# Optimization experiments

Measured on AMD Instinct MI355X. Metric: run time of the kernel, lower is better.

Reference implementation:

```python
import jax, jax.numpy as jnp
from jax import lax
import numpy as np

LRELU_SLOPE = 0.2
DEMOD_EPS = 1e-8


def _mod_conv(x, style, weight, bias, demodulate, pad):
    """StyleGAN2 modulated conv via grouped conv (groups = batch).
    x: [B,Cin,H,W]; style: [B,Cin]; weight: [Cout,Cin,kh,kw]; bias: [Cout]."""
    B, Cin, H, W = x.shape
    Cout, _, kh, kw = weight.shape
    # per-sample modulated weight [B,Cout,Cin,kh,kw]
    wt = weight[None] * style[:, None, :, None, None]
    if demodulate:
        wt = wt / jnp.sqrt(jnp.sum(wt ** 2, axis=(2, 3, 4), keepdims=True) + DEMOD_EPS)
    out = lax.conv_general_dilated(
        x.reshape(1, B * Cin, H, W),
        wt.reshape(B * Cout, Cin, kh, kw),
        window_strides=(1, 1),
        padding=[(pad, pad), (pad, pad)],
        dimension_numbers=('NCHW', 'OIHW', 'NCHW'),
        feature_group_count=B,
    )
    return out.reshape(B, Cout, H, W) + bias[None, :, None, None]


def setup_inputs() -> dict:
    key = jax.random.key(0)
    ks = jax.random.split(key, 16)
    B, Cin, Cout, Wd, H = 4, 512, 256, 512, 64
    f32 = jnp.float32
    d = {
        'x': jax.random.normal(ks[0], (B, Cin, H, H), f32),
        'w': jax.random.normal(ks[1], (B, Wd), f32),
        # conv1: Cin->Cout 3x3
        'w1': jax.random.normal(ks[2], (Cout, Cin, 3, 3), f32) / np.float32(np.sqrt(Cin * 9)),
        'b1': jax.random.normal(ks[3], (Cout,), f32) * 0.01,
        'a1w': jax.random.normal(ks[4], (Cin, Wd), f32) / np.float32(np.sqrt(Wd)),
        'a1b': jnp.ones((Cin,), f32),
        # conv2: Cout->Cout 3x3
        'w2': jax.random.normal(ks[5], (Cout, Cout, 3, 3), f32) / np.float32(np.sqrt(Cout * 9)),
        'b2': jax.random.normal(ks[6], (Cout,), f32) * 0.01,
        'a2w': jax.random.normal(ks[7], (Cout, Wd), f32) / np.float32(np.sqrt(Wd)),
        'a2b': jnp.ones((Cout,), f32),
        # to_rgb: Cout->3 1x1, no demodulation
        'w3': jax.random.normal(ks[8], (3, Cout, 1, 1), f32) / np.float32(np.sqrt(Cout)),
        'b3': jax.random.normal(ks[9], (3,), f32) * 0.01,
        'a3w': jax.random.normal(ks[10], (Cout, Wd), f32) / np.float32(np.sqrt(Wd)),
        'a3b': jnp.ones((Cout,), f32),
    }
    return d


def reference(x, w, w1, b1, a1w, a1b, w2, b2, a2w, a2b, w3, b3, a3w, a3b):
    B, C, H, W = x.shape
    # nn.Upsample(scale_factor=2, mode='bilinear', align_corners=False) == half-pixel bilinear
    xu = jax.image.resize(x, (B, C, 2 * H, 2 * W), method='bilinear')
    s1 = w @ a1w.T + a1b                      # affine -> per-sample style [B,Cin]
    h = jax.nn.leaky_relu(_mod_conv(xu, s1, w1, b1, True, 1), LRELU_SLOPE)
    s2 = w @ a2w.T + a2b
    h = jax.nn.leaky_relu(_mod_conv(h, s2, w2, b2, True, 1), LRELU_SLOPE)
    s3 = w @ a3w.T + a3b
    rgb = jax.nn.leaky_relu(_mod_conv(h, s3, w3, b3, False, 0), LRELU_SLOPE)
    return (h, rgb)
```

## Files before the change

kernel.cpp:

```cpp
#include <hip/hip_runtime.h>
#include <stdint.h>

typedef __attribute__((ext_vector_type(8))) short bhalf8;
typedef __attribute__((ext_vector_type(4))) float fx4;

__device__ __forceinline__ unsigned short f2bf(float f) {
    unsigned u = __builtin_bit_cast(unsigned, f);
    unsigned r = (u + 0x7fffu + ((u >> 16) & 1u)) >> 16;
    return (unsigned short)r;
}
__device__ __forceinline__ float bf2f(unsigned short h) {
    unsigned u = ((unsigned)h) << 16;
    return __builtin_bit_cast(float, u);
}
__device__ __forceinline__ float lrelu(float v) { return v > 0.f ? v : 0.2f * v; }

typedef __attribute__((address_space(1))) void as1_void;
typedef __attribute__((address_space(3))) void as3_void;
__device__ __forceinline__ void gl_lds16(const void* g, void* l) {
    __builtin_amdgcn_global_load_lds((as1_void*)(void*)g, (as3_void*)l, 16, 0, 0);
}

__global__ __launch_bounds__(256) void style_kernel(
    const float* __restrict__ w,
    const float* __restrict__ a1w, const float* __restrict__ a1b,
    const float* __restrict__ a2w, const float* __restrict__ a2b,
    const float* __restrict__ a3w, const float* __restrict__ a3b,
    float* __restrict__ s1, float* __restrict__ s2, float* __restrict__ s3)
{
    int gw = blockIdx.x * 4 + (threadIdx.x >> 6);
    int lane = threadIdx.x & 63;
    int b = gw >> 10, r = gw & 1023;
    const float* arow; const float* abias; float* dst;
    if (r < 512)      { arow = a1w + (size_t)r * 512;        abias = a1b + r;       dst = s1 + b * 512 + r; }
    else if (r < 768) { int rr = r - 512; arow = a2w + (size_t)rr * 512; abias = a2b + rr; dst = s2 + b * 256 + rr; }
    else              { int rr = r - 768; arow = a3w + (size_t)rr * 512; abias = a3b + rr; dst = s3 + b * 256 + rr; }
    const float* wrow = w + b * 512;
    float acc = 0.f;
    #pragma unroll
    for (int j = 0; j < 8; ++j) {
        int c = lane + j * 64;
        acc += wrow[c] * arow[c];
    }
    #pragma unroll
    for (int off = 32; off; off >>= 1) acc += __shfl_down(acc, off, 64);
    if (lane == 0) *dst = acc + *abias;
}

__global__ __launch_bounds__(256) void demod_kernel(
    const float* __restrict__ w1, const float* __restrict__ w2,
    const float* __restrict__ s1, const float* __restrict__ s2,
    float* __restrict__ d1, float* __restrict__ d2)
{
    int blk = blockIdx.x;
    int conv = blk >> 10, b = (blk >> 8) & 3, o = blk & 255;
    int t = threadIdx.x;
    int cin = conv ? 256 : 512;
    const float* s = conv ? (s2 + b * 256) : (s1 + b * 512);
    const float* row = (conv ? w2 : w1) + (size_t)o * cin * 9;
    __shared__ float sv[512];
    for (int i = t; i < cin; i += 256) { float v = s[i]; sv[i] = v * v; }
    __syncthreads();
    float sum = 0.f;
    int n = cin * 9;
    for (int k = t; k < n; k += 256) {
        float v = row[k];
        sum += v * v * sv[k / 9];
    }
    #pragma unroll
    for (int off = 32; off; off >>= 1) sum += __shfl_down(sum, off, 64);
    __shared__ float red[4];
    if ((t & 63) == 0) red[t >> 6] = sum;
    __syncthreads();
    if (t == 0) {
        float tot = red[0] + red[1] + red[2] + red[3];
        (conv ? d2 : d1)[b * 256 + o] = rsqrtf(tot + 1e-8f);
    }
}

__global__ __launch_bounds__(256) void pack_kernel(
    const float* __restrict__ w1, const float* __restrict__ w2,
    unsigned short* __restrict__ wp1, unsigned short* __restrict__ wp2)
{
    int tid = blockIdx.x * 256 + threadIdx.x;
    const int N1 = 1179648, N2 = 589824;
    if (tid < N1) {
        int e = tid & 7, m = (tid >> 3) & 127, kh = (tid >> 10) & 3;
        int dx = (tid >> 12) % 3, ic = (tid / 12288) & 15;
        int dy = (tid / 196608) % 3, mblk = tid / 589824;
        int o = mblk * 128 + m, ci = ic * 32 + kh * 8 + e;
        wp1[tid] = f2bf(w1[((size_t)o * 512 + ci) * 9 + dy * 3 + dx]);
    } else if (tid < N1 + N2) {
        int t2 = tid - N1;
        int e = t2 & 7, m = (t2 >> 3) & 127, kh = (t2 >> 10) & 3;
        int dx = (t2 >> 12) % 3, ic = (t2 / 12288) & 7;
        int dy = (t2 / 98304) % 3, mblk = t2 / 294912;
        int o = mblk * 128 + m, ci = ic * 32 + kh * 8 + e;
        wp2[t2] = f2bf(w2[((size_t)o * 256 + ci) * 9 + dy * 3 + dx]);
    }
}

__global__ __launch_bounds__(256) void upsample_kernel(
    const float* __restrict__ x, const float* __restrict__ s1,
    unsigned short* __restrict__ xu)
{
    __shared__ float Lt[3][64][68];
    const int bid = blockIdx.x;
    const int cch = bid & 7, k = (bid >> 3) & 63, b = bid >> 9;
    const int c0 = cch * 64;
    const int t = threadIdx.x;

    {
        const int px4 = t & 15, cc4 = t >> 4;
        #pragma unroll
        for (int r = 0; r < 3; ++r) {
            int sy = k - 1 + r; sy = sy < 0 ? 0 : (sy > 63 ? 63 : sy);
            float4 v[4];
            #pragma unroll
            for (int j = 0; j < 4; ++j)
                v[j] = *(const float4*)&x[((size_t)(b * 512 + c0 + cc4 * 4 + j) * 64 + sy) * 64 + px4 * 4];
            #pragma unroll
            for (int o = 0; o < 4; ++o) {
                fx4 w4;
                w4[0] = ((const float*)&v[0])[o];
                w4[1] = ((const float*)&v[1])[o];
                w4[2] = ((const float*)&v[2])[o];
                w4[3] = ((const float*)&v[3])[o];
                *(fx4*)&Lt[r][px4 * 4 + o][cc4 * 4] = w4;
            }
        }
    }
    __syncthreads();

    const int oct = t & 7, xob = t >> 3;
    float sty[8];
    #pragma unroll
    for (int j = 0; j < 8; ++j) sty[j] = s1[b * 512 + c0 + oct * 8 + j];

    #pragma unroll
    for (int half = 0; half < 2; ++half) {
        const int yo = 2 * k + half;
        const int rA = half ? 1 : 0, rB = rA + 1;
        const float wyA = half ? 0.75f : 0.25f, wyB = half ? 0.25f : 0.75f;
        #pragma unroll
        for (int i = 0; i < 4; ++i) {
            const int xo = xob + i * 32;
            const int kk = xo >> 1;
            int sx0, sx1; float wx0, wx1;
            if ((xo & 1) == 0) { sx0 = kk > 0 ? kk - 1 : 0; sx1 = kk; wx0 = 0.25f; wx1 = 0.75f; }
            else               { sx0 = kk; sx1 = kk < 63 ? kk + 1 : 63; wx0 = 0.75f; wx1 = 0.25f; }
            unsigned pk[4];
            #pragma unroll
            for (int h = 0; h < 2; ++h) {
                const fx4 a0 = *(const fx4*)&Lt[rA][sx0][oct * 8 + h * 4];
                const fx4 a1 = *(const fx4*)&Lt[rA][sx1][oct * 8 + h * 4];
                const fx4 b0 = *(const fx4*)&Lt[rB][sx0][oct * 8 + h * 4];
                const fx4 b1 = *(const fx4*)&Lt[rB][sx1][oct * 8 + h * 4];
                #pragma unroll
                for (int j2 = 0; j2 < 2; ++j2) {
                    float v0 = wyA * (wx0 * a0[j2 * 2]     + wx1 * a1[j2 * 2])
                             + wyB * (wx0 * b0[j2 * 2]     + wx1 * b1[j2 * 2]);
                    float v1 = wyA * (wx0 * a0[j2 * 2 + 1] + wx1 * a1[j2 * 2 + 1])
                             + wyB * (wx0 * b0[j2 * 2 + 1] + wx1 * b1[j2 * 2 + 1]);
                    v0 *= sty[h * 4 + j2 * 2];
                    v1 *= sty[h * 4 + j2 * 2 + 1];
                    pk[h * 2 + j2] = (unsigned)f2bf(v0) | ((unsigned)f2bf(v1) << 16);
                }
            }
            *(int4*)&xu[((size_t)(b * 128 + yo) * 128 + xo) * 512 + c0 + oct * 8] =
                make_int4(pk[0], pk[1], pk[2], pk[3]);
        }
    }
}

template<int CIN, bool IS_CONV2>
__global__ __launch_bounds__(512, 4) void conv3x3_kernel(
    const unsigned short* __restrict__ inp,
    const unsigned short* __restrict__ wpack,
    const float* __restrict__ dvec,
    const float* __restrict__ bias,
    const float* __restrict__ post,
    unsigned short* __restrict__ outmod,
    float* __restrict__ outf)
{
    constexpr int NIC = CIN / 32;
    __shared__ __attribute__((aligned(16))) short Alds[2][12288];
    __shared__ __attribute__((aligned(16))) short Blds[4][128][32];
    const int tid = threadIdx.x;
    const int lane = tid & 63;
    const int wvi = tid >> 6;
    const int bid = blockIdx.x;
    const int y0 = (bid & 63) << 1;
    const int mblk = (bid >> 6) & 1;
    const int b = bid >> 7;
    const int wm = (wvi >> 2) * 64;
    const int row = (wvi >> 1) & 1;
    const int wn = (wvi & 1) * 64;
    const int lhi = lane >> 4;
    const int llo = lane & 15;

    const int xg = tid >> 2, i8 = tid & 3;
    const int i8s = i8 ^ ((xg >> 1) & 3);

    fx4 acc[4][4];
    #pragma unroll
    for (int mt = 0; mt < 4; ++mt)
        #pragma unroll
        for (int nt = 0; nt < 4; ++nt) acc[mt][nt] = (fx4){0.f, 0.f, 0.f, 0.f};

    auto stageB = [&](int ic) {
        #pragma unroll
        for (int rr = 0; rr < 4; ++rr) {
            const int yy = y0 - 1 + rr;
            char* dstB = (char*)&Blds[rr][0][0] + tid * 16;
            if ((unsigned)yy < 128u) {
                gl_lds16(inp + ((size_t)(b * 128 + yy) * 128 + xg) * CIN + ic * 32 + i8s * 8, dstB);
            } else {
                *(int4*)dstB = make_int4(0, 0, 0, 0);
            }
        }
    };
    auto stageA = [&](int ic, int dy, int buf) {
        const unsigned short* asrc = wpack + ((size_t)(mblk * 3 + dy) * NIC + ic) * 12288;
        #pragma unroll
        for (int j = 0; j < 3; ++j) {
            int g = tid + j * 512;
            gl_lds16(asrc + (size_t)g * 8, (char*)&Alds[buf][0] + g * 16);
        }
    };

    stageB(0);
    stageA(0, 0, 0);
    __syncthreads();

    int par = 0;
    for (int ic = 0; ic < NIC; ++ic) {
        #pragma unroll
        for (int dy = 0; dy < 3; ++dy) {
            const bool last = (ic == NIC - 1) && (dy == 2);
            if (!last) {
                const int nic = (dy == 2) ? ic + 1 : ic;
                const int ndy = (dy == 2) ? 0 : dy + 1;
                stageA(nic, ndy, par ^ 1);
            }
            const short* Ab = &Alds[par][0];
            const short* Brow = &Blds[row + dy][0][0];
            #pragma unroll
            for (int dx = 0; dx < 3; ++dx) {
                bhalf8 af[4], bfr[4];
                #pragma unroll
                for (int mt = 0; mt < 4; ++mt)
                    af[mt] = *(const bhalf8*)&Ab[dx * 4096 + (lhi * 128 + wm + mt * 16 + llo) * 8];
                #pragma unroll
                for (int nt = 0; nt < 4; ++nt) {
                    const int s = wn + nt * 16 + llo + dx;
                    if ((nt == 0 && dx == 0) || (nt == 3 && dx == 2)) {
                        const bool edge = (s == 0) || (s == 129);
                        const int sp = edge ? 0 : (s - 1);
                        const int key = (sp >> 1) & 3;
                        bhalf8 v = *(const bhalf8*)&Brow[sp * 32 + ((lhi ^ key) << 3)];
                        bhalf8 z = {0, 0, 0, 0, 0, 0, 0, 0};
                        bfr[nt] = edge ? z : v;
                    } else {
                        const int sp = s - 1;
                        const int key = (sp >> 1) & 3;
                        bfr[nt] = *(const bhalf8*)&Brow[sp * 32 + ((lhi ^ key) << 3)];
                    }
                }
                __builtin_amdgcn_s_setprio(1);
                #pragma unroll
                for (int mt = 0; mt < 4; ++mt)
                    #pragma unroll
                    for (int nt = 0; nt < 4; ++nt)
                        acc[mt][nt] = __builtin_amdgcn_mfma_f32_16x16x32_bf16(
                            af[mt], bfr[nt], acc[mt][nt], 0, 0, 0);
                __builtin_amdgcn_s_setprio(0);
            }
            if (dy == 2 && ic + 1 < NIC) {
                __syncthreads();
                stageB(ic + 1);
            }
            if (!last) __syncthreads();
            par ^= 1;
        }
    }

    const int y = y0 + row;
    #pragma unroll
    for (int mt = 0; mt < 4; ++mt) {
        const int o0 = mblk * 128 + wm + mt * 16 + lhi * 4;
        const fx4 d4 = *(const fx4*)(dvec + b * 256 + o0);
        const fx4 bb4 = *(const fx4*)(bias + o0);
        const fx4 p4 = *(const fx4*)(post + b * 256 + o0);
        #pragma unroll
        for (int nt = 0; nt < 4; ++nt) {
            const int xo = wn + nt * 16 + llo;
            unsigned lo = 0, hi = 0;
            #pragma unroll
            for (int r = 0; r < 4; ++r) {
                float v = acc[mt][nt][r] * d4[r] + bb4[r];
                v = lrelu(v);
                if (IS_CONV2)
                    outf[(((size_t)b * 256 + o0 + r) * 128 + y) * 128 + xo] = v;
                unsigned short ub = f2bf(v * p4[r]);
                if (r < 2) lo |= (unsigned)ub << (16 * r);
                else       hi |= (unsigned)ub << (16 * (r - 2));
            }
            *(uint2*)&outmod[((size_t)(b * 128 + y) * 128 + xo) * 256 + o0] = make_uint2(lo, hi);
        }
    }
}

__global__ __launch_bounds__(256) void rgb_kernel(
    const unsigned short* __restrict__ hs3,
    const float* __restrict__ w3, const float* __restrict__ b3,
    float* __restrict__ out)
{
    __shared__ float wl[768];
    int t = threadIdx.x;
    for (int i = t; i < 768; i += 256) wl[i] = w3[i];
    __syncthreads();
    int p = blockIdx.x * 64 + (t >> 2);
    int q = t & 3;
    const unsigned short* src = hs3 + (size_t)p * 256 + q * 64;
    float a0 = 0.f, a1 = 0.f, a2 = 0.f;
    #pragma unroll
    for (int c8 = 0; c8 < 64; c8 += 8) {
        int4 pk = *(const int4*)(src + c8);
        #pragma unroll
        for (int qq = 0; qq < 4; ++qq) {
            unsigned uu = ((const unsigned*)&pk)[qq];
            float ve = bf2f((unsigned short)(uu & 0xffffu));
            float vo = bf2f((unsigned short)(uu >> 16));
            int c = q * 64 + c8 + qq * 2;
            a0 += ve * wl[c] + vo * wl[c + 1];
            a1 += ve * wl[256 + c] + vo * wl[256 + c + 1];
            a2 += ve * wl[512 + c] + vo * wl[512 + c + 1];
        }
    }
    a0 += __shfl_xor(a0, 1, 64); a0 += __shfl_xor(a0, 2, 64);
    a1 += __shfl_xor(a1, 1, 64); a1 += __shfl_xor(a1, 2, 64);
    a2 += __shfl_xor(a2, 1, 64); a2 += __shfl_xor(a2, 2, 64);
    int b = p >> 14, yx = p & 16383;
    if (q < 3) {
        float v = (q == 0) ? a0 : (q == 1) ? a1 : a2;
        out[((size_t)b * 3 + q) * 16384 + yx] = lrelu(v + b3[q]);
    }
}

extern "C" void kernel_launch(void* const* d_in, const int* in_sizes, int n_in,
                              void* d_out, int out_size, void* d_ws, size_t ws_size,
                              hipStream_t stream) {
    const float* x   = (const float*)d_in[0];
    const float* w   = (const float*)d_in[1];
    const float* w1  = (const float*)d_in[2];
    const float* b1  = (const float*)d_in[3];
    const float* a1w = (const float*)d_in[4];
    const float* a1b = (const float*)d_in[5];
    const float* w2  = (const float*)d_in[6];
    const float* b2  = (const float*)d_in[7];
    const float* a2w = (const float*)d_in[8];
    const float* a2b = (const float*)d_in[9];
    const float* w3  = (const float*)d_in[10];
    const float* b3  = (const float*)d_in[11];
    const float* a3w = (const float*)d_in[12];
    const float* a3b = (const float*)d_in[13];

    char* ws = (char*)d_ws;
    unsigned short* xu  = (unsigned short*)(ws);
    unsigned short* hs3 = (unsigned short*)(ws);
    unsigned short* t1  = (unsigned short*)(ws + 67108864);
    unsigned short* wp1 = (unsigned short*)(ws + 100663296);
    unsigned short* wp2 = (unsigned short*)(ws + 103022592);
    float* s1 = (float*)(ws + 104202240);
    float* s2 = (float*)(ws + 104210432);
    float* s3 = (float*)(ws + 104214528);
    float* d1 = (float*)(ws + 104218624);
    float* d2 = (float*)(ws + 104222720);

    float* h_out   = (float*)d_out;
    float* rgb_out = h_out + 16777216;

    style_kernel<<<1024, 256, 0, stream>>>(w, a1w, a1b, a2w, a2b, a3w, a3b, s1, s2, s3);
    demod_kernel<<<2048, 256, 0, stream>>>(w1, w2, s1, s2, d1, d2);
    pack_kernel<<<6912, 256, 0, stream>>>(w1, w2, wp1, wp2);
    upsample_kernel<<<2048, 256, 0, stream>>>(x, s1, xu);
    conv3x3_kernel<512, false><<<512, 512, 0, stream>>>(xu, wp1, d1, b1, s2, t1, nullptr);
    conv3x3_kernel<256, true><<<512, 512, 0, stream>>>(t1, wp2, d2, b2, s3, hs3, h_out);
    rgb_kernel<<<1024, 256, 0, stream>>>(hs3, w3, b3, rgb_out);
}
```

Before: 361.9 us.

## Pipeline conv weight/input staging per dx with vmcnt-counted waits and ring buffers

Result: slower. 792.3 us (+118.9%).

```diff
diff --git a/kernel.cpp b/kernel.cpp
--- a/kernel.cpp
+++ b/kernel.cpp
@@ -184,8 +184,8 @@
     float* __restrict__ outf)
 {
     constexpr int NIC = CIN / 32;
-    __shared__ __attribute__((aligned(16))) short Alds[2][12288];
-    __shared__ __attribute__((aligned(16))) short Blds[4][128][32];
+    __shared__ __attribute__((aligned(16))) short Alds[3][4096];
+    __shared__ __attribute__((aligned(16))) short Blds[6][128][32];
     const int tid = threadIdx.x;
     const int lane = tid & 63;
     const int wvi = tid >> 6;
@@ -198,59 +198,91 @@
     const int wn = (wvi & 1) * 64;
     const int lhi = lane >> 4;
     const int llo = lane & 15;
+    const int e0 = (y0 == 0) ? 1 : 0;
+    const int e1 = (y0 == 126) ? 1 : 0;
 
     const int xg = tid >> 2, i8 = tid & 3;
     const int i8s = i8 ^ ((xg >> 1) & 3);
 
+#define WAITVM(N) asm volatile("s_waitcnt vmcnt(" #N ") lgkmcnt(0)" ::: "memory")
+#define CBAR()    asm volatile("" ::: "memory")
+
+    auto stageA1 = [&](int qic, int qdy, int qdx, int slot) {
+        const unsigned short* asrc = wpack + ((size_t)(mblk * 3 + qdy) * NIC + qic) * 12288
+                                           + qdx * 4096;
+        gl_lds16(asrc + (size_t)tid * 8, (char*)&Alds[slot][0] + tid * 16);
+    };
+    auto stageB1 = [&](int icn, int rr, int slot) {
+        const int yy = y0 - 1 + rr;
+        char* dstB = (char*)&Blds[slot][0][0] + tid * 16;
+        if ((unsigned)yy < 128u) {
+            gl_lds16(inp + ((size_t)(b * 128 + yy) * 128 + xg) * CIN + icn * 32 + i8s * 8, dstB);
+        } else {
+            *(int4*)dstB = make_int4(0, 0, 0, 0);
+        }
+    };
+
     fx4 acc[4][4];
     #pragma unroll
     for (int mt = 0; mt < 4; ++mt)
         #pragma unroll
         for (int nt = 0; nt < 4; ++nt) acc[mt][nt] = (fx4){0.f, 0.f, 0.f, 0.f};
 
-    auto stageB = [&](int ic) {
-        #pragma unroll
-        for (int rr = 0; rr < 4; ++rr) {
-            const int yy = y0 - 1 + rr;
-            char* dstB = (char*)&Blds[rr][0][0] + tid * 16;
-            if ((unsigned)yy < 128u) {
-                gl_lds16(inp + ((size_t)(b * 128 + yy) * 128 + xg) * CIN + ic * 32 + i8s * 8, dstB);
-            } else {
-                *(int4*)dstB = make_int4(0, 0, 0, 0);
-            }
-        }
-    };
-    auto stageA = [&](int ic, int dy, int buf) {
-        const unsigned short* asrc = wpack + ((size_t)(mblk * 3 + dy) * NIC + ic) * 12288;
-        #pragma unroll
-        for (int j = 0; j < 3; ++j) {
-            int g = tid + j * 512;
-            gl_lds16(asrc + (size_t)g * 8, (char*)&Alds[buf][0] + g * 16);
-        }
-    };
-
-    stageB(0);
-    stageA(0, 0, 0);
-    __syncthreads();
-
-    int par = 0;
+    stageA1(0, 0, 0, 0); CBAR();
+    stageA1(0, 0, 1, 1); CBAR();
+    stageB1(0, 0, 0); CBAR();
+    stageB1(0, 1, 1); CBAR();
+    stageB1(0, 2, 2); CBAR();
+    stageB1(0, 3, 3); CBAR();
+
+    int bbase = 0;
     for (int ic = 0; ic < NIC; ++ic) {
+        const bool lastic = (ic == NIC - 1);
         #pragma unroll
         for (int dy = 0; dy < 3; ++dy) {
-            const bool last = (ic == NIC - 1) && (dy == 2);
-            if (!last) {
-                const int nic = (dy == 2) ? ic + 1 : ic;
-                const int ndy = (dy == 2) ? 0 : dy + 1;
-                stageA(nic, ndy, par ^ 1);
-            }
-            const short* Ab = &Alds[par][0];
-            const short* Brow = &Blds[row + dy][0][0];
             #pragma unroll
             for (int dx = 0; dx < 3; ++dx) {
+                int n;
+                if (ic == 0 && dy == 0 && dx == 0) n = 2 - e1;
+                else if (lastic) n = (dy == 2 && dx == 2) ? 0 : 1;
+                else if (dx == 0) n = 1;
+                else if (dy == 0) n = 3 - e0;
+                else if (dy == 1) n = 2;
+                else n = 2 - e1;
+                if (n == 0) WAITVM(0);
+                else if (n == 1) WAITVM(1);
+                else if (n == 2) WAITVM(2);
+                else WAITVM(3);
+                __builtin_amdgcn_s_barrier();
+                __builtin_amdgcn_sched_barrier(0);
+                {
+                    const int poff = 3 * dy + dx + 2;
+                    if (!(lastic && dy == 2 && dx >= 1)) {
+                        const int qic = ic + (poff >= 9 ? 1 : 0);
+                        const int qoff = poff >= 9 ? poff - 9 : poff;
+                        stageA1(qic, qoff / 3, qoff % 3, (dx + 2) % 3);
+                        CBAR();
+                    }
+                }
+                if (dx == 0 && !lastic) {
+                    if (dy == 0) {
+                        int s4 = bbase + 4; if (s4 >= 6) s4 -= 6;
+                        int s5 = bbase + 5; if (s5 >= 6) s5 -= 6;
+                        stageB1(ic + 1, 0, s4); CBAR();
+                        stageB1(ic + 1, 1, s5); CBAR();
+                    } else if (dy == 1) {
+                        stageB1(ic + 1, 2, bbase); CBAR();
+                    } else {
+                        int s1b = bbase + 1; if (s1b >= 6) s1b -= 6;
+                        stageB1(ic + 1, 3, s1b); CBAR();
+                    }
+                }
+                int sb = bbase + row + dy; if (sb >= 6) sb -= 6;
+                const short* Brow = &Blds[sb][0][0];
                 bhalf8 af[4], bfr[4];
                 #pragma unroll
                 for (int mt = 0; mt < 4; ++mt)
-                    af[mt] = *(const bhalf8*)&Ab[dx * 4096 + (lhi * 128 + wm + mt * 16 + llo) * 8];
+                    af[mt] = *(const bhalf8*)&Alds[dx][(lhi * 128 + wm + mt * 16 + llo) * 8];
                 #pragma unroll
                 for (int nt = 0; nt < 4; ++nt) {
                     const int s = wn + nt * 16 + llo + dx;
@@ -276,14 +308,11 @@
                             af[mt], bfr[nt], acc[mt][nt], 0, 0, 0);
                 __builtin_amdgcn_s_setprio(0);
             }
-            if (dy == 2 && ic + 1 < NIC) {
-                __syncthreads();
-                stageB(ic + 1);
-            }
-            if (!last) __syncthreads();
-            par ^= 1;
-        }
-    }
+        }
+        bbase += 4; if (bbase >= 6) bbase -= 6;
+    }
+#undef WAITVM
+#undef CBAR
 
     const int y = y0 + row;
     #pragma unroll
```

## Fuse to_rgb 1x1 projection into conv2 epilogue with atomic partial sums

Applied to the files above, without the earlier changes.

Measured after the change: 354.7 us. 1.02x faster.

```diff
diff --git a/kernel.cpp b/kernel.cpp
--- a/kernel.cpp
+++ b/kernel.cpp
@@ -181,7 +181,9 @@
     const float* __restrict__ bias,
     const float* __restrict__ post,
     unsigned short* __restrict__ outmod,
-    float* __restrict__ outf)
+    float* __restrict__ outf,
+    const float* __restrict__ w3,
+    float* __restrict__ rgbpart)
 {
     constexpr int NIC = CIN / 32;
     __shared__ __attribute__((aligned(16))) short Alds[2][12288];
@@ -286,66 +288,73 @@
     }
 
     const int y = y0 + row;
-    #pragma unroll
-    for (int mt = 0; mt < 4; ++mt) {
-        const int o0 = mblk * 128 + wm + mt * 16 + lhi * 4;
-        const fx4 d4 = *(const fx4*)(dvec + b * 256 + o0);
-        const fx4 bb4 = *(const fx4*)(bias + o0);
-        const fx4 p4 = *(const fx4*)(post + b * 256 + o0);
+    if constexpr (!IS_CONV2) {
+        #pragma unroll
+        for (int mt = 0; mt < 4; ++mt) {
+            const int o0 = mblk * 128 + wm + mt * 16 + lhi * 4;
+            const fx4 d4 = *(const fx4*)(dvec + b * 256 + o0);
+            const fx4 bb4 = *(const fx4*)(bias + o0);
+            const fx4 p4 = *(const fx4*)(post + b * 256 + o0);
+            #pragma unroll
+            for (int nt = 0; nt < 4; ++nt) {
+                const int xo = wn + nt * 16 + llo;
+                unsigned lo = 0, hi = 0;
+                #pragma unroll
+                for (int r = 0; r < 4; ++r) {
+                    float v = acc[mt][nt][r] * d4[r] + bb4[r];
+                    v = lrelu(v);
+                    unsigned short ub = f2bf(v * p4[r]);
+                    if (r < 2) lo |= (unsigned)ub << (16 * r);
+                    else       hi |= (unsigned)ub << (16 * (r - 2));
+                }
+                *(uint2*)&outmod[((size_t)(b * 128 + y) * 128 + xo) * 256 + o0] = make_uint2(lo, hi);
+            }
+        }
+    } else {
         #pragma unroll
         for (int nt = 0; nt < 4; ++nt) {
             const int xo = wn + nt * 16 + llo;
-            unsigned lo = 0, hi = 0;
-            #pragma unroll
-            for (int r = 0; r < 4; ++r) {
-                float v = acc[mt][nt][r] * d4[r] + bb4[r];
-                v = lrelu(v);
-                if (IS_CONV2)
+            float pq0 = 0.f, pq1 = 0.f, pq2 = 0.f;
+            #pragma unroll
+            for (int mt = 0; mt < 4; ++mt) {
+                const int o0 = mblk * 128 + wm + mt * 16 + lhi * 4;
+                const fx4 d4 = *(const fx4*)(dvec + b * 256 + o0);
+                const fx4 bb4 = *(const fx4*)(bias + o0);
+                const fx4 p4 = *(const fx4*)(post + b * 256 + o0);
+                const fx4 wq0 = *(const fx4*)(w3 + o0);
+                const fx4 wq1 = *(const fx4*)(w3 + 256 + o0);
+                const fx4 wq2 = *(const fx4*)(w3 + 512 + o0);
+                #pragma unroll
+                for (int r = 0; r < 4; ++r) {
+                    float v = acc[mt][nt][r] * d4[r] + bb4[r];
+                    v = lrelu(v);
                     outf[(((size_t)b * 256 + o0 + r) * 128 + y) * 128 + xo] = v;
-                unsigned short ub = f2bf(v * p4[r]);
-                if (r < 2) lo |= (unsigned)ub << (16 * r);
-                else       hi |= (unsigned)ub << (16 * (r - 2));
-            }
-            *(uint2*)&outmod[((size_t)(b * 128 + y) * 128 + xo) * 256 + o0] = make_uint2(lo, hi);
-        }
-    }
-}
-
-__global__ __launch_bounds__(256) void rgb_kernel(
-    const unsigned short* __restrict__ hs3,
-    const float* __restrict__ w3, const float* __restrict__ b3,
+                    const float hv = v * p4[r];
+                    pq0 += wq0[r] * hv;
+                    pq1 += wq1[r] * hv;
+                    pq2 += wq2[r] * hv;
+                }
+            }
+            pq0 += __shfl_xor(pq0, 16, 64); pq0 += __shfl_xor(pq0, 32, 64);
+            pq1 += __shfl_xor(pq1, 16, 64); pq1 += __shfl_xor(pq1, 32, 64);
+            pq2 += __shfl_xor(pq2, 16, 64); pq2 += __shfl_xor(pq2, 32, 64);
+            if (lhi == 0) {
+                float* rp = rgbpart + (size_t)b * 49152 + (size_t)y * 128 + xo;
+                atomicAdd(rp, pq0);
+                atomicAdd(rp + 16384, pq1);
+                atomicAdd(rp + 32768, pq2);
+            }
+        }
+    }
+}
+
+__global__ __launch_bounds__(256) void rgb_finish_kernel(
+    const float* __restrict__ part, const float* __restrict__ b3,
     float* __restrict__ out)
 {
-    __shared__ float wl[768];
-    int t = threadIdx.x;
-    for (int i = t; i < 768; i += 256) wl[i] = w3[i];
-    __syncthreads();
-    int p = blockIdx.x * 64 + (t >> 2);
-    int q = t & 3;
-    const unsigned short* src = hs3 + (size_t)p * 256 + q * 64;
-    float a0 = 0.f, a1 = 0.f, a2 = 0.f;
-    #pragma unroll
-    for (int c8 = 0; c8 < 64; c8 += 8) {
-        int4 pk = *(const int4*)(src + c8);
-        #pragma unroll
-        for (int qq = 0; qq < 4; ++qq) {
-            unsigned uu = ((const unsigned*)&pk)[qq];
-            float ve = bf2f((unsigned short)(uu & 0xffffu));
-            float vo = bf2f((unsigned short)(uu >> 16));
-            int c = q * 64 + c8 + qq * 2;
-            a0 += ve * wl[c] + vo * wl[c + 1];
-            a1 += ve * wl[256 + c] + vo * wl[256 + c + 1];
-            a2 += ve * wl[512 + c] + vo * wl[512 + c + 1];
-        }
-    }
-    a0 += __shfl_xor(a0, 1, 64); a0 += __shfl_xor(a0, 2, 64);
-    a1 += __shfl_xor(a1, 1, 64); a1 += __shfl_xor(a1, 2, 64);
-    a2 += __shfl_xor(a2, 1, 64); a2 += __shfl_xor(a2, 2, 64);
-    int b = p >> 14, yx = p & 16383;
-    if (q < 3) {
-        float v = (q == 0) ? a0 : (q == 1) ? a1 : a2;
-        out[((size_t)b * 3 + q) * 16384 + yx] = lrelu(v + b3[q]);
-    }
+    int i = blockIdx.x * 256 + threadIdx.x;
+    int q = (i >> 14) % 3;
+    out[i] = lrelu(part[i] + b3[q]);
 }
 
 extern "C" void kernel_launch(void* const* d_in, const int* in_sizes, int n_in,
@@ -368,7 +377,6 @@
 
     char* ws = (char*)d_ws;
     unsigned short* xu  = (unsigned short*)(ws);
-    unsigned short* hs3 = (unsigned short*)(ws);
     unsigned short* t1  = (unsigned short*)(ws + 67108864);
     unsigned short* wp1 = (unsigned short*)(ws + 100663296);
     unsigned short* wp2 = (unsigned short*)(ws + 103022592);
@@ -377,15 +385,17 @@
     float* s3 = (float*)(ws + 104214528);
     float* d1 = (float*)(ws + 104218624);
     float* d2 = (float*)(ws + 104222720);
+    float* rgbpart = (float*)(ws + 104226816);
 
     float* h_out   = (float*)d_out;
     float* rgb_out = h_out + 16777216;
 
+    hipMemsetAsync(rgbpart, 0, 786432, stream);
     style_kernel<<<1024, 256, 0, stream>>>(w, a1w, a1b, a2w, a2b, a3w, a3b, s1, s2, s3);
     demod_kernel<<<2048, 256, 0, stream>>>(w1, w2, s1, s2, d1, d2);
     pack_kernel<<<6912, 256, 0, stream>>>(w1, w2, wp1, wp2);
     upsample_kernel<<<2048, 256, 0, stream>>>(x, s1, xu);
-    conv3x3_kernel<512, false><<<512, 512, 0, stream>>>(xu, wp1, d1, b1, s2, t1, nullptr);
-    conv3x3_kernel<256, true><<<512, 512, 0, stream>>>(t1, wp2, d2, b2, s3, hs3, h_out);
-    rgb_kernel<<<1024, 256, 0, stream>>>(hs3, w3, b3, rgb_out);
-}
+    conv3x3_kernel<512, false><<<512, 512, 0, stream>>>(xu, wp1, d1, b1, s2, t1, nullptr, nullptr, nullptr);
+    conv3x3_kernel<256, true><<<512, 512, 0, stream>>>(t1, wp2, d2, b2, s3, nullptr, h_out, w3, rgbpart);
+    rgb_finish_kernel<<<768, 256, 0, stream>>>(rgbpart, b3, rgb_out);
+}
```
